# Kernel tuning notes

Measured on AMD Instinct MI355X. Metric: run time of the kernel, lower is better.

Reference implementation:

```python
import jax, jax.numpy as jnp
import numpy as np

N_NODES = 50000
N_EDGES = 400000
N_GRAPHS = 256
NUM_TYPES = 200
EMB = 64
HID = 128
HEADS = 4
GDIM = 256  # graph_embed_dim
NUM_CLASSES = 20
EPS = 1e-5
NEG_SLOPE = 0.2


def _gat_conv(h, src, dst, W, a_src, a_dst, bias, heads, out_c, concat):
    """PyG GATConv (with self-loops already appended to src/dst)."""
    n = h.shape[0]
    x = (h @ W.T).reshape(n, heads, out_c)                       # [N,H,C]
    al_s = jnp.einsum('nhc,hc->nh', x, a_src)                    # [N,H]
    al_d = jnp.einsum('nhc,hc->nh', x, a_dst)
    e = jax.nn.leaky_relu(al_s[src] + al_d[dst], NEG_SLOPE)      # [E',H]
    # segment softmax over destination node
    e_max = jax.ops.segment_max(e, dst, num_segments=n)
    e_exp = jnp.exp(e - e_max[dst])
    denom = jax.ops.segment_sum(e_exp, dst, num_segments=n)
    alpha = e_exp / denom[dst]                                   # [E',H]
    out = jax.ops.segment_sum(alpha[:, :, None] * x[src], dst, num_segments=n)  # [N,H,C]
    out = out.reshape(n, heads * out_c) if concat else out.mean(axis=1)
    return out + bias


def _batchnorm(h, gamma, beta):
    # training-mode BatchNorm1d over node dim (biased variance, as torch)
    m = h.mean(axis=0)
    v = jnp.mean((h - m) ** 2, axis=0)
    return (h - m) * jax.lax.rsqrt(v + EPS) * gamma + beta


def setup_inputs() -> dict:
    key = jax.random.key(0)
    ks = jax.random.split(key, 32)
    s = 0.1
    inp = {
        'x': jax.random.randint(ks[0], (N_NODES,), 0, NUM_TYPES),
        'edge_index': jax.random.randint(ks[1], (2, N_EDGES), 0, N_NODES),
        'depth': jax.random.uniform(ks[2], (N_NODES,), jnp.float32),
        'batch': jnp.sort(jax.random.randint(ks[3], (N_NODES,), 0, N_GRAPHS)),
        'emb_table': jax.random.normal(ks[4], (NUM_TYPES, EMB), jnp.float32) * s,
        'depth_w': jax.random.normal(ks[5], (EMB, 1), jnp.float32) * s,
        'depth_b': jnp.zeros((EMB,), jnp.float32),
        'W0': jax.random.normal(ks[6], (HEADS * HID, EMB), jnp.float32) * s,
        'as0': jax.random.normal(ks[7], (HEADS, HID), jnp.float32) * s,
        'ad0': jax.random.normal(ks[8], (HEADS, HID), jnp.float32) * s,
        'b0': jnp.zeros((HEADS * HID,), jnp.float32),
        'g0': jnp.ones((HEADS * HID,), jnp.float32),
        'be0': jnp.zeros((HEADS * HID,), jnp.float32),
        'W1': jax.random.normal(ks[9], (HEADS * HID, HEADS * HID), jnp.float32) * s,
        'as1': jax.random.normal(ks[10], (HEADS, HID), jnp.float32) * s,
        'ad1': jax.random.normal(ks[11], (HEADS, HID), jnp.float32) * s,
        'b1': jnp.zeros((HEADS * HID,), jnp.float32),
        'g1': jnp.ones((HEADS * HID,), jnp.float32),
        'be1': jnp.zeros((HEADS * HID,), jnp.float32),
        # layer 2: 512 -> 128, 1 head, no concat
        'W2': jax.random.normal(ks[12], (GDIM // 2, HEADS * HID), jnp.float32) * s,
        'as2': jax.random.normal(ks[13], (1, GDIM // 2), jnp.float32) * s,
        'ad2': jax.random.normal(ks[14], (1, GDIM // 2), jnp.float32) * s,
        'b2': jnp.zeros((GDIM // 2,), jnp.float32),
        'g2': jnp.ones((GDIM // 2,), jnp.float32),
        'be2': jnp.zeros((GDIM // 2,), jnp.float32),
        # classifier: 256 -> 256 -> 20
        'cw1': jax.random.normal(ks[15], (GDIM, 2 * (GDIM // 2)), jnp.float32) * s,
        'cb1': jnp.zeros((GDIM,), jnp.float32),
        'cw2': jax.random.normal(ks[16], (NUM_CLASSES, GDIM), jnp.float32) * s,
        'cb2': jnp.zeros((NUM_CLASSES,), jnp.float32),
    }
    return inp


def reference(x, edge_index, depth, batch, emb_table, depth_w, depth_b,
              W0, as0, ad0, b0, g0, be0,
              W1, as1, ad1, b1, g1, be1,
              W2, as2, ad2, b2, g2, be2,
              cw1, cb1, cw2, cb2):
    n = x.shape[0]
    # node features: type embedding + depth projection
    h = emb_table[x] + (depth[:, None] @ depth_w.T + depth_b)    # [N,64]
    # add self-loops once (PyG GATConv default add_self_loops=True)
    loop = jnp.arange(n)
    src = jnp.concatenate([edge_index[0], loop])
    dst = jnp.concatenate([edge_index[1], loop])
    layers = [
        (W0, as0, ad0, b0, g0, be0, HEADS, HID, True),
        (W1, as1, ad1, b1, g1, be1, HEADS, HID, True),
        (W2, as2, ad2, b2, g2, be2, 1, GDIM // 2, False),
    ]
    for (W, a_s, a_d, b, g, be, heads, out_c, concat) in layers:
        h = _gat_conv(h, src, dst, W, a_s, a_d, b, heads, out_c, concat)
        h = _batchnorm(h, g, be)
        h = jax.nn.elu(h)
        # dropout: eval mode -> identity
    # global mean / max pooling per graph
    ones = jnp.ones((n,), h.dtype)
    counts = jax.ops.segment_sum(ones, batch, num_segments=N_GRAPHS)
    h_mean = jax.ops.segment_sum(h, batch, num_segments=N_GRAPHS) / jnp.maximum(counts, 1.0)[:, None]
    h_max = jax.ops.segment_max(h, batch, num_segments=N_GRAPHS)
    emb = jnp.concatenate([h_mean, h_max], axis=-1)              # [G,256]
    # classifier (dropout off in eval)
    hidden = jax.nn.relu(emb @ cw1.T + cb1)
    return hidden @ cw2.T + cb2                                  # [G,20]
```

## Files before the change

### kernel.cpp

```cpp
#include <hip/hip_runtime.h>

#define N_NODES 50000
#define N_PAD 50048
#define NBY 391
#define N_EDGES 400000
#define EP (N_EDGES + N_NODES)
#define N_GRAPHS 256
#define EMB 64
#define HID 128
#define HEADS 4
#define GDIM 256
#define NUM_CLASSES 20
#define EPS_BN 1e-5f
#define NEG_SLOPE 0.2f
#define NB_AGG 2048

typedef __attribute__((ext_vector_type(4))) float f32x4;
typedef _Float16 h8 __attribute__((ext_vector_type(8)));
typedef _Float16 h4 __attribute__((ext_vector_type(4)));
typedef _Float16 h2 __attribute__((ext_vector_type(2)));

#define GLD(g, l)                                                              \
    __builtin_amdgcn_global_load_lds(                                          \
        (const __attribute__((address_space(1))) void*)(g),                    \
        (__attribute__((address_space(3))) void*)(l), 16, 0, 0)

__global__ void k_deg(const int* __restrict__ ei, int* __restrict__ deg) {
    int e = blockIdx.x * blockDim.x + threadIdx.x;
    if (e >= EP) return;
    int dst = (e < N_EDGES) ? ei[N_EDGES + e] : (e - N_EDGES);
    atomicAdd(&deg[dst], 1);
}

__global__ void k_scanA(const int* __restrict__ deg, int* __restrict__ incl, int* __restrict__ bsums) {
    __shared__ int sh[1024];
    int t = threadIdx.x;
    int i = blockIdx.x * 1024 + t;
    int v = (i < N_NODES) ? deg[i] : 0;
    int xv = v;
    sh[t] = xv;
    __syncthreads();
    for (int off = 1; off < 1024; off <<= 1) {
        int y = (t >= off) ? sh[t - off] : 0;
        __syncthreads();
        xv += y;
        sh[t] = xv;
        __syncthreads();
    }
    if (i < N_NODES) incl[i] = xv;
    if (t == 1023) bsums[blockIdx.x] = xv;
}

__global__ void k_scanC(const int* __restrict__ incl, const int* __restrict__ deg,
                        const int* __restrict__ bsums, int* __restrict__ offs) {
    int i = blockIdx.x * blockDim.x + threadIdx.x;
    int b = i >> 10;
    int add = 0;
    for (int k = 0; k < b; k++) add += bsums[k];
    if (i < N_NODES) offs[i] = incl[i] - deg[i] + add;
    if (i == 0) offs[N_NODES] = EP;
}

__global__ void k_scatter(const int* __restrict__ ei, const int* __restrict__ offs,
                          int* __restrict__ cnt, int* __restrict__ csr) {
    int e = blockIdx.x * blockDim.x + threadIdx.x;
    if (e >= EP) return;
    int src, dst;
    if (e < N_EDGES) { src = ei[e]; dst = ei[N_EDGES + e]; }
    else { src = e - N_EDGES; dst = src; }
    int pos = atomicAdd(&cnt[dst], 1);
    csr[offs[dst] + pos] = src;
}

__device__ __forceinline__ void cvt1(const float* __restrict__ in, _Float16* __restrict__ o, int i) {
    int f = i * 4;
    float4 v = *(const float4*)(in + f);
    h4 r;
    r[0] = (_Float16)v.x; r[1] = (_Float16)v.y; r[2] = (_Float16)v.z; r[3] = (_Float16)v.w;
    *(h4*)(o + f) = r;
}

__global__ __launch_bounds__(256) void k_setup(const float* __restrict__ W0, const float* __restrict__ as0,
                                               const float* __restrict__ ad0, const float* __restrict__ W1,
                                               const float* __restrict__ W2,
                                               _Float16* __restrict__ W0f, _Float16* __restrict__ W1f,
                                               _Float16* __restrict__ W2f,
                                               float* __restrict__ wtil,
                                               float* __restrict__ bn0, float* __restrict__ bn1,
                                               float* __restrict__ bn2,
                                               int* __restrict__ deg) {
    int b = blockIdx.x, t = threadIdx.x;
    if (b < 256) {
        cvt1(W1, W1f, b * 256 + t);
    } else if (b < 288) {
        cvt1(W0, W0f, (b - 256) * 256 + t);
    } else if (b < 352) {
        cvt1(W2, W2f, (b - 288) * 256 + t);
    } else if (b == 352) {
        int h = t >> 6, k = t & 63;
        float ss = 0.f, sd = 0.f;
        for (int c = 0; c < 128; c++) {
            float w = W0[(size_t)(h * 128 + c) * 64 + k];
            ss += w * as0[h * 128 + c];
            sd += w * ad0[h * 128 + c];
        }
        wtil[t] = ss;
        wtil[256 + t] = sd;
    } else if (b == 353) {
        for (int i = t; i < 1024; i += 256) { bn0[i] = 0.f; bn1[i] = 0.f; bn2[i] = 0.f; }
    } else {
        int i4 = (b - 354) * 256 + t;
        if (i4 < 25000) ((int4*)deg)[i4] = make_int4(0, 0, 0, 0);
    }
}

__global__ __launch_bounds__(256) void k_node_al0(const int* __restrict__ x,
                                                  const float* __restrict__ depth,
                                                  const float* __restrict__ emb_table,
                                                  const float* __restrict__ dw,
                                                  const float* __restrict__ db,
                                                  const float* __restrict__ wtil,
                                                  const int* __restrict__ batch,
                                                  _Float16* __restrict__ h16,
                                                  float* __restrict__ als, float* __restrict__ ald,
                                                  int* __restrict__ goffs) {
    int wid = threadIdx.x >> 6, lane = threadIdx.x & 63;
    int n = blockIdx.x * 4 + wid;
    if (n >= N_NODES) return;
    float v = emb_table[x[n] * EMB + lane] + depth[n] * dw[lane] + db[lane];
    h16[(size_t)n * 64 + lane] = (_Float16)v;
#pragma unroll
    for (int h = 0; h < 4; h++) {
        float ps = v * wtil[h * 64 + lane];
        float pd = v * wtil[256 + h * 64 + lane];
        for (int off = 32; off; off >>= 1) {
            ps += __shfl_xor(ps, off);
            pd += __shfl_xor(pd, off);
        }
        if (lane == 0) { als[n * 4 + h] = ps; ald[n * 4 + h] = pd; }
    }
    if (lane == 0) {
        int b = batch[n];
        int bp = (n == 0) ? -1 : batch[n - 1];
        for (int g = bp + 1; g <= b; g++) goffs[g] = n;
        if (n == N_NODES - 1) {
            for (int g = b + 1; g <= N_GRAPHS; g++) goffs[g] = N_NODES;
        }
    }
}

__global__ __launch_bounds__(256) void k_bnelu(_Float16* __restrict__ a,
                                               const float* __restrict__ sums,
                                               const float* __restrict__ gamma,
                                               const float* __restrict__ beta) {
    const int lane = threadIdx.x & 63;
    const int wid = threadIdx.x >> 6;
    const int c0 = lane * 8;
    const float invN = 1.f / (float)N_NODES;
    float sc[8], sh[8];
#pragma unroll
    for (int k = 0; k < 8; k += 4) {
        float4 s4 = *(const float4*)(sums + c0 + k);
        float4 q4 = *(const float4*)(sums + 512 + c0 + k);
        float4 g4 = *(const float4*)(gamma + c0 + k);
        float4 b4 = *(const float4*)(beta + c0 + k);
        float m, v;
        m = s4.x * invN; v = q4.x * invN - m * m;
        sc[k + 0] = g4.x * __frsqrt_rn(v + EPS_BN); sh[k + 0] = b4.x - m * sc[k + 0];
        m = s4.y * invN; v = q4.y * invN - m * m;
        sc[k + 1] = g4.y * __frsqrt_rn(v + EPS_BN); sh[k + 1] = b4.y - m * sc[k + 1];
        m = s4.z * invN; v = q4.z * invN - m * m;
        sc[k + 2] = g4.z * __frsqrt_rn(v + EPS_BN); sh[k + 2] = b4.z - m * sc[k + 2];
        m = s4.w * invN; v = q4.w * invN - m * m;
        sc[k + 3] = g4.w * __frsqrt_rn(v + EPS_BN); sh[k + 3] = b4.w - m * sc[k + 3];
    }
    const int stride = gridDim.x * 8;
    for (int n = (blockIdx.x * 4 + wid) * 2; n < N_NODES; n += stride) {
        _Float16* p0 = a + (size_t)n * 512 + c0;
        _Float16* p1 = p0 + 512;
        h8 v0 = *(h8*)p0;
        h8 v1 = *(h8*)p1;
        h8 o0, o1;
#pragma unroll
        for (int k = 0; k < 8; k++) {
            float x0 = (float)v0[k] * sc[k] + sh[k];
            x0 = x0 > 0.f ? x0 : expm1f(x0);
            o0[k] = (_Float16)x0;
            float x1 = (float)v1[k] * sc[k] + sh[k];
            x1 = x1 > 0.f ? x1 : expm1f(x1);
            o1[k] = (_Float16)x1;
        }
        *(h8*)p0 = o0;
        *(h8*)p1 = o1;
    }
}

__global__ __launch_bounds__(256) void k_agg0(const _Float16* __restrict__ h16,
                                              const float* __restrict__ als,
                                              const float* __restrict__ ald_g,
                                              const int* __restrict__ offs,
                                              const int* __restrict__ csr,
                                              _Float16* __restrict__ outh) {
    const int lane = threadIdx.x & 63;
    const int wwid = threadIdx.x >> 6;
    const int q = lane >> 4, l = lane & 15;
    const int gw = blockIdx.x * 4 + wwid;
    const int stride = gridDim.x * 16;
    for (int n = gw * 4 + q; n < N_NODES; n += stride) {
        int s0 = offs[n], s1 = offs[n + 1];
        float aldl = (l < 4) ? ald_g[n * 4 + l] : 0.f;
        float acc[4][4] = {};
        float den[4] = {};
        int e = s0;
        for (; e + 4 <= s1; e += 4) {
            int srcA = csr[e], srcB = csr[e + 1];
            int srcC = csr[e + 2], srcD = csr[e + 3];
            float wA = 0.f, wB = 0.f, wC = 0.f, wD = 0.f;
            if (l < 4) {
                float a1 = als[srcA * 4 + l] + aldl;
                a1 = a1 > 0.f ? a1 : NEG_SLOPE * a1;
                wA = expf(a1);
                float a2 = als[srcB * 4 + l] + aldl;
                a2 = a2 > 0.f ? a2 : NEG_SLOPE * a2;
                wB = expf(a2);
                float a3 = als[srcC * 4 + l] + aldl;
                a3 = a3 > 0.f ? a3 : NEG_SLOPE * a3;
                wC = expf(a3);
                float a4 = als[srcD * 4 + l] + aldl;
                a4 = a4 > 0.f ? a4 : NEG_SLOPE * a4;
                wD = expf(a4);
            }
            h4 vA = *(const h4*)(h16 + (size_t)srcA * 64 + l * 4);
            h4 vB = *(const h4*)(h16 + (size_t)srcB * 64 + l * 4);
            h4 vC = *(const h4*)(h16 + (size_t)srcC * 64 + l * 4);
            h4 vD = *(const h4*)(h16 + (size_t)srcD * 64 + l * 4);
            float vA0 = (float)vA[0], vA1 = (float)vA[1], vA2 = (float)vA[2], vA3 = (float)vA[3];
            float vB0 = (float)vB[0], vB1 = (float)vB[1], vB2 = (float)vB[2], vB3 = (float)vB[3];
            float vC0 = (float)vC[0], vC1 = (float)vC[1], vC2 = (float)vC[2], vC3 = (float)vC[3];
            float vD0 = (float)vD[0], vD1 = (float)vD[1], vD2 = (float)vD[2], vD3 = (float)vD[3];
#pragma unroll
            for (int h = 0; h < 4; h++) {
                float whA = __shfl(wA, q * 16 + h);
                float whB = __shfl(wB, q * 16 + h);
                float whC = __shfl(wC, q * 16 + h);
                float whD = __shfl(wD, q * 16 + h);
                den[h] += (whA + whB) + (whC + whD);
                acc[h][0] += whA * vA0 + whB * vB0 + whC * vC0 + whD * vD0;
                acc[h][1] += whA * vA1 + whB * vB1 + whC * vC1 + whD * vD1;
                acc[h][2] += whA * vA2 + whB * vB2 + whC * vC2 + whD * vD2;
                acc[h][3] += whA * vA3 + whB * vB3 + whC * vC3 + whD * vD3;
            }
        }
        for (; e < s1; e++) {
            int src = csr[e];
            float w = 0.f;
            if (l < 4) {
                float a1 = als[src * 4 + l] + aldl;
                a1 = a1 > 0.f ? a1 : NEG_SLOPE * a1;
                w = expf(a1);
            }
            h4 v = *(const h4*)(h16 + (size_t)src * 64 + l * 4);
            float v0 = (float)v[0], v1 = (float)v[1], v2 = (float)v[2], v3 = (float)v[3];
#pragma unroll
            for (int h = 0; h < 4; h++) {
                float wh = __shfl(w, q * 16 + h);
                den[h] += wh;
                acc[h][0] += wh * v0;
                acc[h][1] += wh * v1;
                acc[h][2] += wh * v2;
                acc[h][3] += wh * v3;
            }
        }
#pragma unroll
        for (int h = 0; h < 4; h++) {
            float id = 1.f / den[h];
            h4 hv;
            hv[0] = (_Float16)(acc[h][0] * id);
            hv[1] = (_Float16)(acc[h][1] * id);
            hv[2] = (_Float16)(acc[h][2] * id);
            hv[3] = (_Float16)(acc[h][3] * id);
            *(h4*)(outh + (size_t)n * 256 + h * 64 + l * 4) = hv;
        }
    }
}

__global__ __launch_bounds__(256) void k_gemm0h(const _Float16* __restrict__ A,
                                                const _Float16* __restrict__ W,
                                                const float* __restrict__ bias,
                                                _Float16* __restrict__ outA,
                                                float* __restrict__ bnacc) {
    __shared__ h8 sA[2][512], sW[2][512];
    const int nbx = gridDim.x;
    const int d = blockIdx.y * nbx + blockIdx.x;
    const int by = (d / (8 * nbx)) * 8 + (d & 7);
    const int bx = (d >> 3) % nbx;
    if (by >= NBY) return;
    const int hd = bx;
    const int t = threadIdx.x;
    const int lane = t & 63;
    const int wid = t >> 6;
    const int wm = wid >> 1, wn = wid & 1;
    const int r0 = by * 128;
    const int l15 = lane & 15, quad = lane >> 4;
    f32x4 acc[4][4] = {};
    auto stage = [&](int buf, int kb) {
#pragma unroll
        for (int r = 0; r < 2; r++) {
            int c = r * 256 + t;
            int row = c >> 2, q = c & 3;
            size_t gA = ((size_t)(r0 + row) * 256 + hd * 64 + kb) * 2 + q * 16;
            size_t gW = ((size_t)(hd * 128 + row) * 64 + kb) * 2 + q * 16;
            GLD((const char*)A + gA, (char*)&sA[buf][0] + c * 16);
            GLD((const char*)W + gW, (char*)&sW[buf][0] + c * 16);
        }
    };
    stage(0, 0);
    __syncthreads();
#pragma unroll
    for (int ki = 0; ki < 2; ki++) {
        int cur = ki & 1;
        if (ki + 1 < 2) stage(cur ^ 1, (ki + 1) * 32);
        h8 a[4], w[4];
#pragma unroll
        for (int i = 0; i < 4; i++) {
            a[i] = sA[cur][(wm * 64 + i * 16 + l15) * 4 + quad];
            w[i] = sW[cur][(wn * 64 + i * 16 + l15) * 4 + quad];
        }
#pragma unroll
        for (int i = 0; i < 4; i++)
#pragma unroll
            for (int j = 0; j < 4; j++)
                acc[i][j] = __builtin_amdgcn_mfma_f32_16x16x32_f16(a[i], w[j], acc[i][j], 0, 0, 0);
        __syncthreads();
    }
    float colsum[4] = {}, colsq[4] = {};
#pragma unroll
    for (int i = 0; i < 4; i++) {
        int gr = r0 + wm * 64 + i * 16 + quad * 4;
#pragma unroll
        for (int j = 0; j < 4; j++) {
            int gc = hd * 128 + wn * 64 + j * 16 + l15;
            float bv = bias[gc];
#pragma unroll
            for (int rg = 0; rg < 4; rg++) {
                int rr = gr + rg;
                if (rr < N_NODES) {
                    float o = acc[i][j][rg] + bv;
                    outA[(size_t)rr * 512 + gc] = (_Float16)o;
                    colsum[j] += o;
                    colsq[j] += o * o;
                }
            }
        }
    }
#pragma unroll
    for (int j = 0; j < 4; j++) {
        colsum[j] += __shfl_xor(colsum[j], 16);
        colsum[j] += __shfl_xor(colsum[j], 32);
        colsq[j] += __shfl_xor(colsq[j], 16);
        colsq[j] += __shfl_xor(colsq[j], 32);
    }
    float* sS = (float*)&sA[0][0];
    float* sQ = (float*)&sW[0][0];
    __syncthreads();
    if (quad == 0) {
#pragma unroll
        for (int j = 0; j < 4; j++) {
            int c = wn * 64 + j * 16 + l15;
            sS[c * 2 + wm] = colsum[j];
            sQ[c * 2 + wm] = colsq[j];
        }
    }
    __syncthreads();
    if (t < 128) {
        atomicAdd(bnacc + hd * 128 + t, sS[t * 2] + sS[t * 2 + 1]);
        atomicAdd(bnacc + 512 + hd * 128 + t, sQ[t * 2] + sQ[t * 2 + 1]);
    }
}

__global__ __launch_bounds__(256) void k_gemm_mfma(const _Float16* __restrict__ A,
                                                   const _Float16* __restrict__ W,
                                                   const float* __restrict__ a_src,
                                                   const float* __restrict__ a_dst,
                                                   float* __restrict__ als_g,
                                                   float* __restrict__ ald_g,
                                                   _Float16* __restrict__ out,
                                                   int K, int M, int heads) {
    __shared__ h8 sA[2][512], sW[2][512];
    const int nbx = gridDim.x;
    const int d = blockIdx.y * nbx + blockIdx.x;
    const int by = (d / (8 * nbx)) * 8 + (d & 7);
    const int bx = (d >> 3) % nbx;
    if (by >= NBY) return;
    const int t = threadIdx.x;
    const int lane = t & 63;
    const int wid = t >> 6;
    const int wm = wid >> 1, wn = wid & 1;
    const int r0 = by * 128, c0 = bx * 128;
    const int l15 = lane & 15, quad = lane >> 4;
    f32x4 acc[4][4] = {};
    auto stage = [&](int buf, int kb) {
#pragma unroll
        for (int r = 0; r < 2; r++) {
            int c = r * 256 + t;
            int row = c >> 2, q = c & 3;
            size_t gA = ((size_t)(r0 + row) * K + kb) * 2 + q * 16;
            size_t gW = ((size_t)(c0 + row) * K + kb) * 2 + q * 16;
            GLD((const char*)A + gA, (char*)&sA[buf][0] + c * 16);
            GLD((const char*)W + gW, (char*)&sW[buf][0] + c * 16);
        }
    };
    stage(0, 0);
    __syncthreads();
    const int nkb = K >> 5;
    for (int ki = 0; ki < nkb; ki++) {
        int cur = ki & 1;
        if (ki + 1 < nkb) stage(cur ^ 1, (ki + 1) * 32);
        h8 a[4], w[4];
#pragma unroll
        for (int i = 0; i < 4; i++) {
            a[i] = sA[cur][(wm * 64 + i * 16 + l15) * 4 + quad];
            w[i] = sW[cur][(wn * 64 + i * 16 + l15) * 4 + quad];
        }
#pragma unroll
        for (int i = 0; i < 4; i++)
#pragma unroll
            for (int j = 0; j < 4; j++)
                acc[i][j] = __builtin_amdgcn_mfma_f32_16x16x32_f16(a[i], w[j], acc[i][j], 0, 0, 0);
        __syncthreads();
    }
#pragma unroll
    for (int i = 0; i < 4; i++) {
        int gr = r0 + wm * 64 + i * 16 + quad * 4;
#pragma unroll
        for (int j = 0; j < 4; j++) {
            int gc = c0 + wn * 64 + j * 16 + l15;
#pragma unroll
            for (int rg = 0; rg < 4; rg++) {
                int rr = gr + rg;
                if (rr < N_NODES) out[(size_t)rr * M + gc] = (_Float16)acc[i][j][rg];
            }
        }
    }
    const int hd = bx;
    float ps[4][4] = {}, pd[4][4] = {};
#pragma unroll
    for (int j = 0; j < 4; j++) {
        int ch = wn * 64 + j * 16 + l15;
        float av = a_src[hd * 128 + ch];
        float dv = a_dst[hd * 128 + ch];
#pragma unroll
        for (int i = 0; i < 4; i++)
#pragma unroll
            for (int rg = 0; rg < 4; rg++) {
                ps[i][rg] += acc[i][j][rg] * av;
                pd[i][rg] += acc[i][j][rg] * dv;
            }
    }
#pragma unroll
    for (int m = 1; m < 16; m <<= 1)
#pragma unroll
        for (int i = 0; i < 4; i++)
#pragma unroll
            for (int rg = 0; rg < 4; rg++) {
                ps[i][rg] += __shfl_xor(ps[i][rg], m);
                pd[i][rg] += __shfl_xor(pd[i][rg], m);
            }
    float* sS = (float*)&sA[0][0];
    float* sD = (float*)&sW[0][0];
    if (l15 == 0) {
#pragma unroll
        for (int i = 0; i < 4; i++)
#pragma unroll
            for (int rg = 0; rg < 4; rg++) {
                int ri = wm * 64 + i * 16 + quad * 4 + rg;
                sS[ri * 2 + wn] = ps[i][rg];
                sD[ri * 2 + wn] = pd[i][rg];
            }
    }
    __syncthreads();
    if (t < 128) {
        int row = r0 + t;
        if (row < N_NODES) {
            als_g[row * heads + hd] = sS[t * 2] + sS[t * 2 + 1];
            ald_g[row * heads + hd] = sD[t * 2] + sD[t * 2 + 1];
        }
    }
}

__global__ __launch_bounds__(256) void k_agg512(const _Float16* __restrict__ xf,
                                                const float* __restrict__ als,
                                                const float* __restrict__ ald_g,
                                                const int* __restrict__ offs,
                                                const int* __restrict__ csr,
                                                const float* __restrict__ bias,
                                                _Float16* __restrict__ out16,
                                                float* __restrict__ bnacc) {
    __shared__ float pool[4][1024];
    const int wid = threadIdx.x >> 6, lane = threadIdx.x & 63;
    int* s_src = (int*)&pool[wid][0];
    float* s_w = &pool[wid][64];
    const int gw = blockIdx.x * 4 + wid;
    const int nw = gridDim.x * 4;
    const int hh = lane >> 4;
    const int c0 = lane * 8;
    float bias8[8];
#pragma unroll
    for (int k = 0; k < 8; k++) bias8[k] = bias[c0 + k];
    float bns[8] = {}, bnq[8] = {};
    for (int n = gw; n < N_NODES; n += nw) {
        int s0 = offs[n], s1 = offs[n + 1];
        float4 aldv = *(const float4*)(ald_g + n * 4);
        float a[8] = {};
        float den = 0.f;
        for (int base = s0; base < s1; base += 64) {
            int j = base + lane;
            int srcj = 0;
            float4 alv = make_float4(0.f, 0.f, 0.f, 0.f);
            if (j < s1) {
                srcj = csr[j];
                alv = *(const float4*)(als + srcj * 4);
            }
            float e0 = alv.x + aldv.x; e0 = e0 > 0.f ? e0 : NEG_SLOPE * e0;
            float e1 = alv.y + aldv.y; e1 = e1 > 0.f ? e1 : NEG_SLOPE * e1;
            float e2 = alv.z + aldv.z; e2 = e2 > 0.f ? e2 : NEG_SLOPE * e2;
            float e3 = alv.w + aldv.w; e3 = e3 > 0.f ? e3 : NEG_SLOPE * e3;
            s_src[lane] = srcj;
            s_w[0 * 64 + lane] = expf(e0);
            s_w[1 * 64 + lane] = expf(e1);
            s_w[2 * 64 + lane] = expf(e2);
            s_w[3 * 64 + lane] = expf(e3);
            int cend = min(64, s1 - base);
            int e = 0;
            for (; e + 8 <= cend; e += 8) {
                h8 v[8];
                float w[8];
#pragma unroll
                for (int u = 0; u < 8; u++) {
                    v[u] = *(const h8*)(xf + (size_t)s_src[e + u] * 512 + c0);
                    w[u] = s_w[hh * 64 + e + u];
                }
#pragma unroll
                for (int u = 0; u < 8; u++) {
                    den += w[u];
#pragma unroll
                    for (int k = 0; k < 8; k++) a[k] += w[u] * (float)v[u][k];
                }
            }
            for (; e + 2 <= cend; e += 2) {
                h8 vA = *(const h8*)(xf + (size_t)s_src[e] * 512 + c0);
                h8 vB = *(const h8*)(xf + (size_t)s_src[e + 1] * 512 + c0);
                float wA = s_w[hh * 64 + e], wB = s_w[hh * 64 + e + 1];
                den += wA + wB;
#pragma unroll
                for (int k = 0; k < 8; k++) a[k] += wA * (float)vA[k] + wB * (float)vB[k];
            }
            if (e < cend) {
                h8 v = *(const h8*)(xf + (size_t)s_src[e] * 512 + c0);
                float w = s_w[hh * 64 + e];
                den += w;
#pragma unroll
                for (int k = 0; k < 8; k++) a[k] += w * (float)v[k];
            }
        }
        float id = 1.f / den;
        h8 ov;
#pragma unroll
        for (int k = 0; k < 8; k++) {
            float o = a[k] * id + bias8[k];
            ov[k] = (_Float16)o;
            bns[k] += o;
            bnq[k] += o * o;
        }
        *(h8*)(out16 + (size_t)n * 512 + c0) = ov;
    }
#pragma unroll
    for (int k = 0; k < 8; k++) {
        pool[wid][c0 + k] = bns[k];
        pool[wid][512 + c0 + k] = bnq[k];
    }
    __syncthreads();
    for (int t = threadIdx.x; t < 1024; t += 256)
        atomicAdd(bnacc + t, pool[0][t] + pool[1][t] + pool[2][t] + pool[3][t]);
}

__global__ __launch_bounds__(256) void k_agg128(const _Float16* __restrict__ xf,
                                                const float* __restrict__ als,
                                                const float* __restrict__ ald_g,
                                                const int* __restrict__ offs,
                                                const int* __restrict__ csr,
                                                const float* __restrict__ bias,
                                                _Float16* __restrict__ out_h,
                                                float* __restrict__ bnacc) {
    __shared__ float pool[4][256];
    const int wid = threadIdx.x >> 6, lane = threadIdx.x & 63;
    int* s_src = (int*)&pool[wid][0];
    float* s_w = &pool[wid][64];
    const int gw = blockIdx.x * 4 + wid;
    const int nw = gridDim.x * 4;
    const int c = lane * 2;
    const float2 biasv = *(const float2*)(bias + c);
    float bns0 = 0.f, bns1 = 0.f, bnq0 = 0.f, bnq1 = 0.f;
    for (int n = gw; n < N_NODES; n += nw) {
        int s0 = offs[n], s1 = offs[n + 1];
        float aldv = ald_g[n];
        float ax = 0.f, ay = 0.f, den = 0.f;
        for (int base = s0; base < s1; base += 64) {
            int j = base + lane;
            int srcj = 0;
            float alv = 0.f;
            if (j < s1) { srcj = csr[j]; alv = als[srcj]; }
            float e0 = alv + aldv;
            e0 = e0 > 0.f ? e0 : NEG_SLOPE * e0;
            s_src[lane] = srcj;
            s_w[lane] = expf(e0);
            int cend = min(64, s1 - base);
            int e = 0;
            for (; e + 8 <= cend; e += 8) {
                h2 v[8];
                float w[8];
#pragma unroll
                for (int u = 0; u < 8; u++) {
                    v[u] = *(const h2*)(xf + (size_t)s_src[e + u] * 128 + c);
                    w[u] = s_w[e + u];
                }
#pragma unroll
                for (int u = 0; u < 8; u++) {
                    den += w[u];
                    ax += w[u] * (float)v[u][0];
                    ay += w[u] * (float)v[u][1];
                }
            }
            for (; e < cend; e++) {
                h2 v = *(const h2*)(xf + (size_t)s_src[e] * 128 + c);
                float w = s_w[e];
                den += w;
                ax += w * (float)v[0];
                ay += w * (float)v[1];
            }
        }
        float id = 1.f / den;
        float ox = ax * id + biasv.x;
        float oy = ay * id + biasv.y;
        h2 oh;
        oh[0] = (_Float16)ox;
        oh[1] = (_Float16)oy;
        *(h2*)(out_h + (size_t)n * 128 + c) = oh;
        bns0 += ox; bnq0 += ox * ox;
        bns1 += oy; bnq1 += oy * oy;
    }
    pool[wid][c] = bns0; pool[wid][c + 1] = bns1;
    pool[wid][128 + c] = bnq0; pool[wid][128 + c + 1] = bnq1;
    __syncthreads();
    {
        int t = threadIdx.x;
        atomicAdd(bnacc + t, pool[0][t] + pool[1][t] + pool[2][t] + pool[3][t]);
    }
}

__global__ __launch_bounds__(256) void k_poolclassify(const _Float16* __restrict__ C,
                                                      const float* __restrict__ bnsums,
                                                      const float* __restrict__ gamma,
                                                      const float* __restrict__ beta,
                                                      const int* __restrict__ goffs,
                                                      const float* __restrict__ cw1, const float* __restrict__ cb1,
                                                      const float* __restrict__ cw2, const float* __restrict__ cb2,
                                                      float* __restrict__ out) {
    __shared__ float er[256];
    __shared__ float red[256];
    int g = blockIdx.x, t = threadIdx.x;
    int c = t & 127, half = t >> 7;
    const float invN = 1.f / (float)N_NODES;
    float m = bnsums[c] * invN;
    float var = bnsums[128 + c] * invN - m * m;
    float sc = gamma[c] * __frsqrt_rn(var + EPS_BN);
    float sh = beta[c] - m * sc;
    int s = goffs[g], e = goffs[g + 1];
    float sum = 0.f, mx = -INFINITY;
    for (int n = s + half; n < e; n += 2) {
        float x = (float)C[(size_t)n * 128 + c] * sc + sh;
        x = x > 0.f ? x : expm1f(x);
        sum += x;
        mx = fmaxf(mx, x);
    }
    red[t] = sum;
    __syncthreads();
    float sumT = red[c] + red[128 + c];
    __syncthreads();
    red[t] = mx;
    __syncthreads();
    float mxT = fmaxf(red[c], red[128 + c]);
    int cnt = e - s;
    if (half == 0) {
        er[c] = sumT / (float)max(cnt, 1);
        er[128 + c] = mxT;
    }
    __syncthreads();
    float acc = cb1[t];
    for (int k = 0; k < 256; k++) acc += er[k] * cw1[t * 256 + k];
    __syncthreads();
    red[t] = fmaxf(acc, 0.f);
    __syncthreads();
    if (t < NUM_CLASSES) {
        float o = cb2[t];
        for (int k = 0; k < 256; k++) o += red[k] * cw2[t * 256 + k];
        out[g * NUM_CLASSES + t] = o;
    }
}

extern "C" void kernel_launch(void* const* d_in, const int* in_sizes, int n_in,
                              void* d_out, int out_size, void* d_ws, size_t ws_size,
                              hipStream_t stream) {
    (void)in_sizes; (void)n_in; (void)out_size; (void)ws_size;
    const int* x = (const int*)d_in[0];
    const int* ei = (const int*)d_in[1];
    const float* depth = (const float*)d_in[2];
    const int* batch = (const int*)d_in[3];
    const float* emb_table = (const float*)d_in[4];
    const float* depth_w = (const float*)d_in[5];
    const float* depth_b = (const float*)d_in[6];
    const float* W0 = (const float*)d_in[7];
    const float* as0 = (const float*)d_in[8];
    const float* ad0 = (const float*)d_in[9];
    const float* b0 = (const float*)d_in[10];
    const float* g0 = (const float*)d_in[11];
    const float* be0 = (const float*)d_in[12];
    const float* W1 = (const float*)d_in[13];
    const float* as1 = (const float*)d_in[14];
    const float* ad1 = (const float*)d_in[15];
    const float* b1 = (const float*)d_in[16];
    const float* g1 = (const float*)d_in[17];
    const float* be1 = (const float*)d_in[18];
    const float* W2 = (const float*)d_in[19];
    const float* as2 = (const float*)d_in[20];
    const float* ad2 = (const float*)d_in[21];
    const float* b2 = (const float*)d_in[22];
    const float* g2 = (const float*)d_in[23];
    const float* be2 = (const float*)d_in[24];
    const float* cw1 = (const float*)d_in[25];
    const float* cb1 = (const float*)d_in[26];
    const float* cw2 = (const float*)d_in[27];
    const float* cb2 = (const float*)d_in[28];
    float* out = (float*)d_out;

    size_t off = 0;
    char* base = (char*)d_ws;
    auto carve = [&](size_t bytes) -> void* {
        void* p = base + off;
        off += (bytes + 255) & ~(size_t)255;
        return p;
    };
    float* B = (float*)carve((size_t)N_NODES * 512 * 2);
    _Float16* A16 = (_Float16*)carve((size_t)N_PAD * 512 * 2);
    _Float16* W0f = (_Float16*)carve((size_t)512 * 64 * 2);
    _Float16* W1f = (_Float16*)carve((size_t)512 * 512 * 2);
    _Float16* W2f = (_Float16*)carve((size_t)128 * 512 * 2);
    float* als = (float*)carve((size_t)N_NODES * HEADS * 4);
    float* ald = (float*)carve((size_t)N_NODES * HEADS * 4);
    float* bn0 = (float*)carve(1024 * 4);
    float* bn1 = (float*)carve(1024 * 4);
    float* bn2 = (float*)carve(1024 * 4);
    float* wtil = (float*)carve(512 * 4);
    int* deg = (int*)carve((size_t)2 * N_NODES * 4);
    int* cnt = deg + N_NODES;
    int* incl = (int*)carve((size_t)N_NODES * 4);
    int* offs = (int*)carve((size_t)(N_NODES + 1) * 4);
    int* bsums = (int*)carve(64 * 4);
    int* csr = (int*)carve((size_t)EP * 4);
    int* goffs = (int*)carve((size_t)(N_GRAPHS + 1) * 4);

    _Float16* h16 = (_Float16*)B;
    _Float16* hth = (_Float16*)((char*)B + (size_t)N_NODES * 64 * 2);
    _Float16* Bh = (_Float16*)B;
    _Float16* C = (_Float16*)A16;

    const int TPB = 256;
    int gbN = (N_NODES + TPB - 1) / TPB;
    int gbE = (EP + TPB - 1) / TPB;
    int nbScan = (N_NODES + 1023) / 1024;
    int gbNode4 = (N_NODES + 3) / 4;
    dim3 g512(4, 392);
    dim3 g128(1, 391);

    k_setup<<<452, TPB, 0, stream>>>(W0, as0, ad0, W1, W2, W0f, W1f, W2f, wtil,
                                     bn0, bn1, bn2, deg);
    k_deg<<<gbE, TPB, 0, stream>>>(ei, deg);
    k_scanA<<<nbScan, 1024, 0, stream>>>(deg, incl, bsums);
    k_scanC<<<gbN, TPB, 0, stream>>>(incl, deg, bsums, offs);
    k_scatter<<<gbE, TPB, 0, stream>>>(ei, offs, cnt, csr);

    k_node_al0<<<gbNode4, TPB, 0, stream>>>(x, depth, emb_table, depth_w, depth_b, wtil,
                                            batch, h16, als, ald, goffs);
    k_agg0<<<NB_AGG, TPB, 0, stream>>>(h16, als, ald, offs, csr, hth);
    k_gemm0h<<<g512, TPB, 0, stream>>>(hth, W0f, b0, A16, bn0);
    k_bnelu<<<2048, TPB, 0, stream>>>(A16, bn0, g0, be0);
    k_gemm_mfma<<<g512, TPB, 0, stream>>>(A16, W1f, as1, ad1, als, ald, Bh, 512, 512, HEADS);
    k_agg512<<<NB_AGG, TPB, 0, stream>>>(Bh, als, ald, offs, csr, b1, A16, bn1);
    k_bnelu<<<2048, TPB, 0, stream>>>(A16, bn1, g1, be1);
    k_gemm_mfma<<<g128, TPB, 0, stream>>>(A16, W2f, as2, ad2, als, ald, Bh, 512, 128, 1);
    k_agg128<<<NB_AGG, TPB, 0, stream>>>(Bh, als, ald, offs, csr, b2, C, bn2);
    k_poolclassify<<<N_GRAPHS, TPB, 0, stream>>>(C, bn2, g2, be2, goffs, cw1, cb1, cw2, cb2, out);
}
```

Before: 583.4 us.

## Quantize layer-1 GAT features to int8 with per-head scales for aggregation

The layer-1 GEMM epilogue now computes a per-row, per-head absmax, stores int8 features plus fp16 scales, and the 512-wide aggregation gathers int8 rows, folding the scale into the attention weight. This halves the bytes gathered per edge in the memory-bound neighbor aggregation. It adds reduction and scalar byte stores to the GEMM epilogue and introduces quantization error in the layer output.

```diff
diff --git a/kernel.cpp b/kernel.cpp
--- a/kernel.cpp
+++ b/kernel.cpp
@@ -19,6 +19,7 @@
 typedef _Float16 h8 __attribute__((ext_vector_type(8)));
 typedef _Float16 h4 __attribute__((ext_vector_type(4)));
 typedef _Float16 h2 __attribute__((ext_vector_type(2)));
+typedef signed char c8 __attribute__((ext_vector_type(8)));
 
 #define GLD(g, l)                                                              \
     __builtin_amdgcn_global_load_lds(                                          \
@@ -378,6 +379,153 @@
     }
 }
 
+__global__ __launch_bounds__(256) void k_gemm_q8(const _Float16* __restrict__ A,
+                                                 const _Float16* __restrict__ W,
+                                                 const float* __restrict__ a_src,
+                                                 const float* __restrict__ a_dst,
+                                                 float* __restrict__ als_g,
+                                                 float* __restrict__ ald_g,
+                                                 signed char* __restrict__ out8,
+                                                 _Float16* __restrict__ scl,
+                                                 int K, int M, int heads) {
+    __shared__ h8 sA[2][512], sW[2][512];
+    const int nbx = gridDim.x;
+    const int d = blockIdx.y * nbx + blockIdx.x;
+    const int by = (d / (8 * nbx)) * 8 + (d & 7);
+    const int bx = (d >> 3) % nbx;
+    if (by >= NBY) return;
+    const int t = threadIdx.x;
+    const int lane = t & 63;
+    const int wid = t >> 6;
+    const int wm = wid >> 1, wn = wid & 1;
+    const int r0 = by * 128, c0 = bx * 128;
+    const int l15 = lane & 15, quad = lane >> 4;
+    f32x4 acc[4][4] = {};
+    auto stage = [&](int buf, int kb) {
+#pragma unroll
+        for (int r = 0; r < 2; r++) {
+            int c = r * 256 + t;
+            int row = c >> 2, q = c & 3;
+            size_t gA = ((size_t)(r0 + row) * K + kb) * 2 + q * 16;
+            size_t gW = ((size_t)(c0 + row) * K + kb) * 2 + q * 16;
+            GLD((const char*)A + gA, (char*)&sA[buf][0] + c * 16);
+            GLD((const char*)W + gW, (char*)&sW[buf][0] + c * 16);
+        }
+    };
+    stage(0, 0);
+    __syncthreads();
+    const int nkb = K >> 5;
+    for (int ki = 0; ki < nkb; ki++) {
+        int cur = ki & 1;
+        if (ki + 1 < nkb) stage(cur ^ 1, (ki + 1) * 32);
+        h8 a[4], w[4];
+#pragma unroll
+        for (int i = 0; i < 4; i++) {
+            a[i] = sA[cur][(wm * 64 + i * 16 + l15) * 4 + quad];
+            w[i] = sW[cur][(wn * 64 + i * 16 + l15) * 4 + quad];
+        }
+#pragma unroll
+        for (int i = 0; i < 4; i++)
+#pragma unroll
+            for (int j = 0; j < 4; j++)
+                acc[i][j] = __builtin_amdgcn_mfma_f32_16x16x32_f16(a[i], w[j], acc[i][j], 0, 0, 0);
+        __syncthreads();
+    }
+    float* sAm = (float*)&sA[0][0];
+    {
+        float amax[4][4];
+#pragma unroll
+        for (int i = 0; i < 4; i++)
+#pragma unroll
+            for (int rg = 0; rg < 4; rg++) {
+                float m = 0.f;
+#pragma unroll
+                for (int j = 0; j < 4; j++) m = fmaxf(m, fabsf(acc[i][j][rg]));
+#pragma unroll
+                for (int mk = 1; mk < 16; mk <<= 1) m = fmaxf(m, __shfl_xor(m, mk));
+                amax[i][rg] = m;
+            }
+        if (l15 == 0) {
+#pragma unroll
+            for (int i = 0; i < 4; i++)
+#pragma unroll
+                for (int rg = 0; rg < 4; rg++) {
+                    int ri = wm * 64 + i * 16 + quad * 4 + rg;
+                    sAm[ri * 2 + wn] = amax[i][rg];
+                }
+        }
+    }
+    __syncthreads();
+#pragma unroll
+    for (int i = 0; i < 4; i++) {
+        int gr = r0 + wm * 64 + i * 16 + quad * 4;
+#pragma unroll
+        for (int rg = 0; rg < 4; rg++) {
+            int ri = wm * 64 + i * 16 + quad * 4 + rg;
+            float amax = fmaxf(sAm[ri * 2], sAm[ri * 2 + 1]);
+            _Float16 s_h = (_Float16)(amax * (1.f / 127.f));
+            float s_r = (float)s_h;
+            float inv = s_r > 0.f ? 1.f / s_r : 0.f;
+            int rr = gr + rg;
+            if (rr < N_NODES) {
+                if (wn == 0 && l15 == 0) scl[(size_t)rr * 4 + bx] = s_h;
+#pragma unroll
+                for (int j = 0; j < 4; j++) {
+                    int gc = c0 + wn * 64 + j * 16 + l15;
+                    int q = (int)rintf(acc[i][j][rg] * inv);
+                    q = q > 127 ? 127 : (q < -127 ? -127 : q);
+                    out8[(size_t)rr * 512 + gc] = (signed char)q;
+                }
+            }
+        }
+    }
+    __syncthreads();
+    const int hd = bx;
+    float ps[4][4] = {}, pd[4][4] = {};
+#pragma unroll
+    for (int j = 0; j < 4; j++) {
+        int ch = wn * 64 + j * 16 + l15;
+        float av = a_src[hd * 128 + ch];
+        float dv = a_dst[hd * 128 + ch];
+#pragma unroll
+        for (int i = 0; i < 4; i++)
+#pragma unroll
+            for (int rg = 0; rg < 4; rg++) {
+                ps[i][rg] += acc[i][j][rg] * av;
+                pd[i][rg] += acc[i][j][rg] * dv;
+            }
+    }
+#pragma unroll
+    for (int m = 1; m < 16; m <<= 1)
+#pragma unroll
+        for (int i = 0; i < 4; i++)
+#pragma unroll
+            for (int rg = 0; rg < 4; rg++) {
+                ps[i][rg] += __shfl_xor(ps[i][rg], m);
+                pd[i][rg] += __shfl_xor(pd[i][rg], m);
+            }
+    float* sS = (float*)&sA[0][0];
+    float* sD = (float*)&sW[0][0];
+    if (l15 == 0) {
+#pragma unroll
+        for (int i = 0; i < 4; i++)
+#pragma unroll
+            for (int rg = 0; rg < 4; rg++) {
+                int ri = wm * 64 + i * 16 + quad * 4 + rg;
+                sS[ri * 2 + wn] = ps[i][rg];
+                sD[ri * 2 + wn] = pd[i][rg];
+            }
+    }
+    __syncthreads();
+    if (t < 128) {
+        int row = r0 + t;
+        if (row < N_NODES) {
+            als_g[row * heads + hd] = sS[t * 2] + sS[t * 2 + 1];
+            ald_g[row * heads + hd] = sD[t * 2] + sD[t * 2 + 1];
+        }
+    }
+}
+
 __global__ __launch_bounds__(256) void k_gemm_mfma(const _Float16* __restrict__ A,
                                                    const _Float16* __restrict__ W,
                                                    const float* __restrict__ a_src,
@@ -488,7 +636,8 @@
     }
 }
 
-__global__ __launch_bounds__(256) void k_agg512(const _Float16* __restrict__ xf,
+__global__ __launch_bounds__(256) void k_agg512(const signed char* __restrict__ x8,
+                                                const _Float16* __restrict__ scl,
                                                 const float* __restrict__ als,
                                                 const float* __restrict__ ald_g,
                                                 const int* __restrict__ offs,
@@ -533,34 +682,41 @@
             int cend = min(64, s1 - base);
             int e = 0;
             for (; e + 8 <= cend; e += 8) {
-                h8 v[8];
-                float w[8];
+                c8 v[8];
+                float w[8], ws[8];
 #pragma unroll
                 for (int u = 0; u < 8; u++) {
-                    v[u] = *(const h8*)(xf + (size_t)s_src[e + u] * 512 + c0);
+                    int s = s_src[e + u];
+                    v[u] = *(const c8*)(x8 + (size_t)s * 512 + c0);
                     w[u] = s_w[hh * 64 + e + u];
+                    ws[u] = w[u] * (float)scl[(size_t)s * 4 + hh];
                 }
 #pragma unroll
                 for (int u = 0; u < 8; u++) {
                     den += w[u];
 #pragma unroll
-                    for (int k = 0; k < 8; k++) a[k] += w[u] * (float)v[u][k];
+                    for (int k = 0; k < 8; k++) a[k] += ws[u] * (float)v[u][k];
                 }
             }
             for (; e + 2 <= cend; e += 2) {
-                h8 vA = *(const h8*)(xf + (size_t)s_src[e] * 512 + c0);
-                h8 vB = *(const h8*)(xf + (size_t)s_src[e + 1] * 512 + c0);
+                int sa = s_src[e], sb = s_src[e + 1];
+                c8 vA = *(const c8*)(x8 + (size_t)sa * 512 + c0);
+                c8 vB = *(const c8*)(x8 + (size_t)sb * 512 + c0);
                 float wA = s_w[hh * 64 + e], wB = s_w[hh * 64 + e + 1];
+                float wsA = wA * (float)scl[(size_t)sa * 4 + hh];
+                float wsB = wB * (float)scl[(size_t)sb * 4 + hh];
                 den += wA + wB;
 #pragma unroll
-                for (int k = 0; k < 8; k++) a[k] += wA * (float)vA[k] + wB * (float)vB[k];
+                for (int k = 0; k < 8; k++) a[k] += wsA * (float)vA[k] + wsB * (float)vB[k];
             }
             if (e < cend) {
-                h8 v = *(const h8*)(xf + (size_t)s_src[e] * 512 + c0);
+                int s = s_src[e];
+                c8 v = *(const c8*)(x8 + (size_t)s * 512 + c0);
                 float w = s_w[hh * 64 + e];
+                float ws = w * (float)scl[(size_t)s * 4 + hh];
                 den += w;
 #pragma unroll
-                for (int k = 0; k < 8; k++) a[k] += w * (float)v[k];
+                for (int k = 0; k < 8; k++) a[k] += ws * (float)v[k];
             }
         }
         float id = 1.f / den;
@@ -771,6 +927,8 @@
 
     _Float16* h16 = (_Float16*)B;
     _Float16* hth = (_Float16*)((char*)B + (size_t)N_NODES * 64 * 2);
+    signed char* X8 = (signed char*)B;
+    _Float16* scl = (_Float16*)((char*)B + (26u << 20));
     _Float16* Bh = (_Float16*)B;
     _Float16* C = (_Float16*)A16;
 
@@ -794,8 +952,8 @@
     k_agg0<<<NB_AGG, TPB, 0, stream>>>(h16, als, ald, offs, csr, hth);
     k_gemm0h<<<g512, TPB, 0, stream>>>(hth, W0f, b0, A16, bn0);
     k_bnelu<<<2048, TPB, 0, stream>>>(A16, bn0, g0, be0);
-    k_gemm_mfma<<<g512, TPB, 0, stream>>>(A16, W1f, as1, ad1, als, ald, Bh, 512, 512, HEADS);
-    k_agg512<<<NB_AGG, TPB, 0, stream>>>(Bh, als, ald, offs, csr, b1, A16, bn1);
+    k_gemm_q8<<<g512, TPB, 0, stream>>>(A16, W1f, as1, ad1, als, ald, X8, scl, 512, 512, HEADS);
+    k_agg512<<<NB_AGG, TPB, 0, stream>>>(X8, scl, als, ald, offs, csr, b1, A16, bn1);
     k_bnelu<<<2048, TPB, 0, stream>>>(A16, bn1, g1, be1);
     k_gemm_mfma<<<g128, TPB, 0, stream>>>(A16, W2f, as2, ad2, als, ald, Bh, 512, 128, 1);
     k_agg128<<<NB_AGG, TPB, 0, stream>>>(Bh, als, ald, offs, csr, b2, C, bn2);
```

Measured after the change: 579.7 us. Within noise of the previous version (-0.6%).
